# Optimization experiments

Hardware: AMD Instinct MI355X
Metric: run time of the kernel (lower is better)

Reference implementation:

```python
import jax, jax.numpy as jnp
import numpy as np

# static config (matches init_kwargs)
P = 16          # proj_patch_dim (window size)
F = 128         # fmap_dim
NH = F // P     # windows per side = 8
N = P * P       # tokens per window = 256
H = 8           # attn_heads
A = 32          # attn_dim (head dim)
C = 32          # leff_filters_out (channels)
INNER = 128     # leff_filters
B = 8           # batch
EPS = 1e-5

# relative-position index (static)
_c = np.stack(np.meshgrid(np.arange(P), np.arange(P), indexing='ij'))  # [2,P,P]
_f = _c.reshape(2, -1)                                                  # [2,N]
_r = _f[:, :, None] - _f[:, None, :]                                    # [2,N,N]
_rpi = (_r[0] + P - 1) * (2 * P - 1) + (_r[1] + P - 1)                  # [N,N]
RPI = jnp.asarray(_rpi.reshape(-1))

# shifted-window attention mask (static)
_sm = np.zeros((F, F), np.float32)
_cnt = 0
_slices = (slice(0, -P), slice(-P, -P // 2), slice(-P // 2, None))
for _hs in _slices:
    for _ws in _slices:
        _sm[_hs, _ws] = _cnt
        _cnt += 1
_smw = _sm.reshape(NH, P, NH, P).transpose(0, 2, 1, 3).reshape(NH * NH, N)
_am = _smw[:, None, :] - _smw[:, :, None]
_am = np.where(_am != 0, np.float32(-100.0), np.float32(0.0))
SHIFT_MASK = jnp.asarray(_am.reshape(1, NH * NH, 1, N, N))


def _ln(x, g, b):
    m = jnp.mean(x, axis=-1, keepdims=True)
    v = jnp.var(x, axis=-1, keepdims=True)
    return (x - m) / jnp.sqrt(v + EPS) * g + b


def setup_inputs() -> dict:
    key = jax.random.key(0)
    ks = jax.random.split(key, 16)
    s = 0.02
    return {
        'x': jax.random.normal(ks[0], (B, F * F, C), jnp.float32),
        'norm1_g': jnp.ones((C,), jnp.float32),
        'norm1_b': jnp.zeros((C,), jnp.float32),
        'mod_w': jax.random.normal(ks[1], (N, C), jnp.float32) * s,
        'qkv_w': jax.random.normal(ks[2], (C, 3 * H * A), jnp.float32) * s,
        'qkv_b': jnp.zeros((3 * H * A,), jnp.float32),
        'rpbt': jax.random.normal(ks[3], ((2 * P - 1) ** 2, H), jnp.float32) * s,
        'rev_w': jax.random.normal(ks[4], (H * A, C), jnp.float32) * s,
        'rev_b': jnp.zeros((C,), jnp.float32),
        'norm2_g': jnp.ones((C,), jnp.float32),
        'norm2_b': jnp.zeros((C,), jnp.float32),
        'lp1_w': jax.random.normal(ks[5], (C, INNER), jnp.float32) * s,
        'lp1_b': jnp.zeros((INNER,), jnp.float32),
        'conv_w': jax.random.normal(ks[6], (3, 3, INNER, INNER), jnp.float32) * s,  # HWIO
        'conv_b': jnp.zeros((INNER,), jnp.float32),
        'lp2_w': jax.random.normal(ks[7], (INNER, C), jnp.float32) * s,
        'lp2_b': jnp.zeros((C,), jnp.float32),
    }


def reference(x, norm1_g, norm1_b, mod_w, qkv_w, qkv_b, rpbt, rev_w, rev_b,
              norm2_g, norm2_b, lp1_w, lp1_b, conv_w, conv_b, lp2_w, lp2_b):
    shortcut = x
    h = _ln(x, norm1_g, norm1_b)
    h = h.reshape(B, F, F, C)
    h = jnp.roll(h, (-P // 2, -P // 2), axis=(1, 2))          # cyclic shift
    # window partition: [B*NH*NH, N, C]
    h = h.reshape(B, NH, P, NH, P, C).transpose(0, 1, 3, 2, 4, 5).reshape(B * NH * NH, N, C)
    h = h + mod_w                                              # learned modulator
    qkv = h @ qkv_w + qkv_b                                    # [W, N, 3*H*A]
    qkv = qkv.reshape(-1, N, 3, H, A).transpose(2, 0, 3, 1, 4) # [3, W, H, N, A]
    q = qkv[0] * (A ** -0.5)
    k = qkv[1]
    v = qkv[2]
    attn = jnp.einsum('whna,whma->whnm', q, k)                 # [W, H, N, N]
    rpb = rpbt[RPI].reshape(N, N, H).transpose(2, 0, 1)        # [H, N, N]
    attn = attn + rpb[None]
    attn = attn.reshape(B, NH * NH, H, N, N) + SHIFT_MASK
    attn = attn.reshape(-1, H, N, N)
    attn = jax.nn.softmax(attn, axis=-1)
    o = jnp.einsum('whnm,whma->whna', attn, v)                 # [W, H, N, A]
    o = o.transpose(0, 2, 1, 3).reshape(-1, N, H * A)
    o = o @ rev_w + rev_b                                      # [W, N, C]
    # window reverse + reverse cyclic shift
    o = o.reshape(B, NH, NH, P, P, C).transpose(0, 1, 3, 2, 4, 5).reshape(B, F, F, C)
    o = jnp.roll(o, (P // 2, P // 2), axis=(1, 2)).reshape(B, F * F, C)
    x_res = shortcut + o
    # LeFF
    y = _ln(x_res, norm2_g, norm2_b)
    y = jax.nn.gelu(y @ lp1_w + lp1_b, approximate=False)
    y = y.reshape(B, F, F, INNER)
    y = jax.lax.conv_general_dilated(y, conv_w, (1, 1), 'SAME',
                                     dimension_numbers=('NHWC', 'HWIO', 'NHWC')) + conv_b
    y = jax.nn.gelu(y, approximate=False)
    y = y.reshape(B, F * F, INNER)
    y = jax.nn.gelu(y @ lp2_w + lp2_b, approximate=False)
    return y + x_res
```

## Files before the change

### kernel.cpp

```cpp
#include <hip/hip_runtime.h>
#include <math.h>

#define Fdim 128
#define Pw   16
#define Hh   8
#define Cc   32
#define Bb   8

typedef short  short8  __attribute__((ext_vector_type(8)));
typedef float  floatx4 __attribute__((ext_vector_type(4)));

#define QSC   0.17677669529663688f
#define MASKC (-100.0f)

__device__ __forceinline__ float gelu_f(float x){
    return 0.5f * x * (1.0f + erff(x * 0.70710678118654752f));
}
__device__ __forceinline__ unsigned pk2(float a, float b){
    unsigned ua = (__builtin_bit_cast(unsigned, a) + 0x8000u) >> 16;
    unsigned ub = (__builtin_bit_cast(unsigned, b) + 0x8000u) & 0xffff0000u;
    return ua | ub;
}
__device__ __forceinline__ short bf16s(float a){
    return (short)((__builtin_bit_cast(unsigned, a) + 0x8000u) >> 16);
}
__device__ __forceinline__ float hi2f(unsigned d){ return __builtin_bit_cast(float, d & 0xffff0000u); }
__device__ __forceinline__ float lo2f(unsigned d){ return __builtin_bit_cast(float, d << 16); }

__global__ __launch_bounds__(256) void prep_kernel(
    const float* __restrict__ qkv_w, const float* __restrict__ rev_w,
    const float* __restrict__ rpbt,  const float* __restrict__ lp1_w,
    const float* __restrict__ conv_w, const float* __restrict__ lp2_w,
    short* __restrict__ qkv_wT, short* __restrict__ rev_wT, unsigned* __restrict__ rplb,
    short* __restrict__ lp1_wT, short* __restrict__ conv_wT, short* __restrict__ lp2_wT)
{
    int i = blockIdx.x * 256 + threadIdx.x;
    if (i < 24576){
        int col = i >> 5, c = i & 31;
        qkv_wT[i] = bf16s(qkv_w[c*768 + col]);
    } else if (i < 32768){
        int j = i - 24576;
        int h = j >> 10, r = j & 1023;
        int c = r >> 5, a = r & 31;
        rev_wT[j] = bf16s(rev_w[(h*32 + a)*32 + c]);
    } else if (i < 40464){
        int j = i - 32768;
        int h = j / 962, d = j % 962;
        int g0 = (d < 481) ? (2*d) : (2*(d-481) + 1);
        float f0 = (g0     < 961) ? rpbt[g0*8 + h]     : 0.f;
        float f1 = (g0 + 1 < 961) ? rpbt[(g0+1)*8 + h] : 0.f;
        rplb[j] = pk2(f0, f1);
    } else if (i < 44560){
        int j = i - 40464;
        int f = j >> 5, c = j & 31;
        lp1_wT[j] = bf16s(lp1_w[c*128 + f]);
    } else if (i < 192016){
        int j = i - 44560;
        int cil = j & 31, co = (j >> 5) & 127, s = j >> 12;
        int tap = s % 9, kc = s / 9;
        conv_wT[j] = bf16s(conv_w[(tap*128 + kc*32 + cil)*128 + co]);
    } else if (i < 196112){
        int j = i - 192016;
        int oc = j >> 7, co = j & 127;
        lp2_wT[j] = bf16s(lp2_w[co*32 + oc]);
    }
}

__global__ __launch_bounds__(256, 2) void attn_kernel(
    const float* __restrict__ x,   const float* __restrict__ n1g,
    const float* __restrict__ n1b, const float* __restrict__ mod_w,
    const float* __restrict__ qkv_b, const float* __restrict__ rev_b,
    const short* __restrict__ qkv_wT, const short* __restrict__ rev_wT,
    const unsigned* __restrict__ rplb,
    float* __restrict__ x_res)
{
    __shared__ __align__(16) short hmodS[256*32];
    __shared__ __align__(16) short Kbuf[256*40];
    __shared__ __align__(16) short Qbuf[256*40];
    __shared__ __align__(16) short VTb[32*264];
    __shared__ __align__(16) unsigned rplbS[962];
    __shared__ unsigned regnp[64];

    const int w  = blockIdx.x;
    const int b  = w >> 6;
    const int wi = w & 63;
    const int wh = wi >> 3, ww = wi & 7;
    const int tid  = threadIdx.x;
    const int wv   = tid >> 6;
    const int ln   = tid & 63;
    const int quad = ln >> 4;
    const int l15  = ln & 15;
    const bool masked = (wh == 7) || (ww == 7);

    {
        const int n  = tid;
        const int rn = n >> 4, cn = n & 15;
        const int gh = (wh*Pw + rn + 8) & 127;
        const int gw = (ww*Pw + cn + 8) & 127;
        const float* xr = x + (((size_t)b << 14) + (gh << 7) + gw) * Cc;
        float v[Cc];
        const float4* x4 = reinterpret_cast<const float4*>(xr);
        float4* v4 = reinterpret_cast<float4*>(v);
        #pragma unroll
        for (int i = 0; i < Cc/4; i++) v4[i] = x4[i];
        float mean = 0.f;
        #pragma unroll
        for (int c = 0; c < Cc; c++) mean += v[c];
        mean *= (1.0f/Cc);
        float var = 0.f;
        #pragma unroll
        for (int c = 0; c < Cc; c++){ float d = v[c] - mean; var = fmaf(d, d, var); }
        var *= (1.0f/Cc);
        const float rinv = rsqrtf(var + 1e-5f);
        #pragma unroll
        for (int c = 0; c < Cc; c++)
            v[c] = (v[c] - mean)*rinv*n1g[c] + n1b[c] + mod_w[n*Cc + c];
        #pragma unroll
        for (int i = 0; i < 4; i++){
            uint4 dw;
            dw.x = pk2(v[8*i+0], v[8*i+1]);
            dw.y = pk2(v[8*i+2], v[8*i+3]);
            dw.z = pk2(v[8*i+4], v[8*i+5]);
            dw.w = pk2(v[8*i+6], v[8*i+7]);
            *(uint4*)(&hmodS[n*32 + i*8]) = dw;
        }
    }
    if (tid < 64){
        int rm  = tid >> 2;
        int shm = wh*Pw + rm;
        int hreg = (shm < 112) ? 0 : ((shm < 120) ? 1 : 2);
        unsigned dw = 0;
        #pragma unroll
        for (int i = 0; i < 4; i++){
            int cm  = (tid & 3)*4 + i;
            int swm = ww*Pw + cm;
            int wreg = (swm < 112) ? 0 : ((swm < 120) ? 1 : 2);
            dw |= (unsigned)(hreg*3 + wreg) << (8*i);
        }
        regnp[tid] = dw;
    }
    __syncthreads();

    unsigned regq[4] = {0,0,0,0};
    if (masked){
        #pragma unroll
        for (int nt = 0; nt < 4; nt++){
            int q = wv*64 + nt*16 + l15;
            regq[nt] = (regnp[q >> 2] >> ((q & 3)*8)) & 255u;
        }
    }

    floatx4 RV[2][4];
    #pragma unroll
    for (int cm = 0; cm < 2; cm++)
        #pragma unroll
        for (int nt = 0; nt < 4; nt++)
            RV[cm][nt] = (floatx4){0.f,0.f,0.f,0.f};

    const int s0lane = 12 + l15 - 4*quad;
    const floatx4 zz = (floatx4){0.f,0.f,0.f,0.f};

    for (int h = 0; h < Hh; h++){
        __syncthreads();

        #pragma unroll
        for (int k2 = 0; k2 < 4; k2++){
            int i = k2*256 + tid;
            if (i < 962) rplbS[i] = rplb[h*962 + i];
        }

        short8 HA[4];
        #pragma unroll
        for (int i = 0; i < 4; i++)
            HA[i] = *(const short8*)(&hmodS[(wv*64 + i*16 + l15)*32 + quad*8]);
        short8 WB[3][2]; float bias[3][2];
        #pragma unroll
        for (int m = 0; m < 3; m++)
            #pragma unroll
            for (int nt = 0; nt < 2; nt++){
                int col = m*256 + h*32 + nt*16 + l15;
                WB[m][nt]  = *(const short8*)(qkv_wT + col*32 + quad*8);
                bias[m][nt] = qkv_b[col];
            }
        #pragma unroll
        for (int i = 0; i < 4; i++){
            int tokbase = wv*64 + i*16 + quad*4;
            #pragma unroll
            for (int nt = 0; nt < 2; nt++){
                int col = nt*16 + l15;
                floatx4 qf = __builtin_amdgcn_mfma_f32_16x16x32_bf16(HA[i], WB[0][nt], zz, 0,0,0);
                floatx4 kf = __builtin_amdgcn_mfma_f32_16x16x32_bf16(HA[i], WB[1][nt], zz, 0,0,0);
                floatx4 vf = __builtin_amdgcn_mfma_f32_16x16x32_bf16(HA[i], WB[2][nt], zz, 0,0,0);
                float bq = bias[0][nt], bk = bias[1][nt], bv = bias[2][nt];
                #pragma unroll
                for (int r = 0; r < 4; r++){
                    Qbuf[(tokbase + r)*40 + col] = bf16s((qf[r] + bq)*QSC);
                    Kbuf[(tokbase + r)*40 + col] = bf16s(kf[r] + bk);
                }
                uint2 vv;
                vv.x = pk2(vf[0] + bv, vf[1] + bv);
                vv.y = pk2(vf[2] + bv, vf[3] + bv);
                *(uint2*)(&VTb[col*264 + tokbase]) = vv;
            }
        }
        __syncthreads();

        short8 QB[4];
        #pragma unroll
        for (int nt = 0; nt < 4; nt++)
            QB[nt] = *(const short8*)(&Qbuf[(wv*64 + nt*16 + l15)*40 + quad*8]);

        floatx4 OT[2][4];
        #pragma unroll
        for (int am = 0; am < 2; am++)
            #pragma unroll
            for (int nt = 0; nt < 4; nt++)
                OT[am][nt] = (floatx4){0.f,0.f,0.f,0.f};
        float rs[4] = {0.f,0.f,0.f,0.f};

        for (int ch = 0; ch < 8; ch++){
            short8 KA[2];
            KA[0] = *(const short8*)(&Kbuf[(ch*32 +      l15)*40 + quad*8]);
            KA[1] = *(const short8*)(&Kbuf[(ch*32 + 16 + l15)*40 + quad*8]);

            unsigned pd0[5], pd1[5];
            int base = wv*4 - ch*2;
            #pragma unroll
            for (int j = 0; j < 5; j++){
                int dt  = base + j - 1;
                int g0  = (dt + 15)*31 + s0lane;
                int dwi = (g0 & 1) ? (481 + (g0 >> 1)) : (g0 >> 1);
                pd0[j] = rplbS[dwi];
                pd1[j] = rplbS[dwi + 1];
            }
            unsigned rk[2] = {0,0};
            if (masked){
                rk[0] = regnp[ch*8 +     quad];
                rk[1] = regnp[ch*8 + 4 + quad];
            }

            floatx4 S[2][4];
            #pragma unroll
            for (int sub = 0; sub < 2; sub++)
                #pragma unroll
                for (int nt = 0; nt < 4; nt++)
                    S[sub][nt] = __builtin_amdgcn_mfma_f32_16x16x32_bf16(KA[sub], QB[nt], zz, 0,0,0);

            #pragma unroll
            for (int sub = 0; sub < 2; sub++)
                #pragma unroll
                for (int nt = 0; nt < 4; nt++){
                    int j = nt - sub + 1;
                    float e0 = S[sub][nt][0] + hi2f(pd1[j]);
                    float e1 = S[sub][nt][1] + lo2f(pd1[j]);
                    float e2 = S[sub][nt][2] + hi2f(pd0[j]);
                    float e3 = S[sub][nt][3] + lo2f(pd0[j]);
                    if (masked){
                        e0 += (((rk[sub]      ) & 255u) == regq[nt]) ? 0.f : MASKC;
                        e1 += (((rk[sub] >>  8) & 255u) == regq[nt]) ? 0.f : MASKC;
                        e2 += (((rk[sub] >> 16) & 255u) == regq[nt]) ? 0.f : MASKC;
                        e3 += (((rk[sub] >> 24) & 255u) == regq[nt]) ? 0.f : MASKC;
                    }
                    float p0 = __expf(e0), p1 = __expf(e1);
                    float p2 = __expf(e2), p3 = __expf(e3);
                    rs[nt] += (p0 + p1) + (p2 + p3);
                    uint2 pv; pv.x = pk2(p0, p1); pv.y = pk2(p2, p3);
                    *(uint2*)(&Qbuf[(wv*64 + nt*16 + l15)*40 + sub*16 + quad*4]) = pv;
                }

            short8 VA0 = *(const short8*)(&VTb[(     l15)*264 + ch*32 + quad*8]);
            short8 VA1 = *(const short8*)(&VTb[(16 + l15)*264 + ch*32 + quad*8]);
            #pragma unroll
            for (int nt = 0; nt < 4; nt++){
                short8 PB = *(const short8*)(&Qbuf[(wv*64 + nt*16 + l15)*40 + quad*8]);
                OT[0][nt] = __builtin_amdgcn_mfma_f32_16x16x32_bf16(VA0, PB, OT[0][nt], 0,0,0);
                OT[1][nt] = __builtin_amdgcn_mfma_f32_16x16x32_bf16(VA1, PB, OT[1][nt], 0,0,0);
            }
        }

        float inv[4];
        #pragma unroll
        for (int nt = 0; nt < 4; nt++){
            float t = rs[nt] + __shfl_xor(rs[nt], 16, 64);
            t = t + __shfl_xor(t, 32, 64);
            inv[nt] = 1.0f / t;
        }
        #pragma unroll
        for (int am = 0; am < 2; am++)
            #pragma unroll
            for (int nt = 0; nt < 4; nt++){
                floatx4 o = OT[am][nt];
                float iv = inv[nt];
                uint2 ov;
                ov.x = pk2(o[0]*iv, o[1]*iv);
                ov.y = pk2(o[2]*iv, o[3]*iv);
                *(uint2*)(&Qbuf[(wv*64 + nt*16 + l15)*40 + am*16 + quad*4]) = ov;
            }

        short8 RA0 = *(const short8*)(rev_wT + h*1024 + (     l15)*32 + quad*8);
        short8 RA1 = *(const short8*)(rev_wT + h*1024 + (16 + l15)*32 + quad*8);
        #pragma unroll
        for (int nt = 0; nt < 4; nt++){
            short8 OB = *(const short8*)(&Qbuf[(wv*64 + nt*16 + l15)*40 + quad*8]);
            RV[0][nt] = __builtin_amdgcn_mfma_f32_16x16x32_bf16(RA0, OB, RV[0][nt], 0,0,0);
            RV[1][nt] = __builtin_amdgcn_mfma_f32_16x16x32_bf16(RA1, OB, RV[1][nt], 0,0,0);
        }
    }

    #pragma unroll
    for (int cm = 0; cm < 2; cm++){
        float4 rb = *(const float4*)(rev_b + cm*16 + quad*4);
        #pragma unroll
        for (int nt = 0; nt < 4; nt++){
            int gh = (wh*Pw + wv*4 + nt + 8) & 127;
            int gw = (ww*Pw + l15 + 8) & 127;
            size_t gaddr = (((size_t)b << 14) + (gh << 7) + gw)*Cc + cm*16 + quad*4;
            float4 xv = *(const float4*)(x + gaddr);
            floatx4 o = RV[cm][nt];
            float4 ov;
            ov.x = xv.x + rb.x + o[0];
            ov.y = xv.y + rb.y + o[1];
            ov.z = xv.z + rb.z + o[2];
            ov.w = xv.w + rb.w + o[3];
            *(float4*)(x_res + gaddr) = ov;
        }
    }
}

__global__ __launch_bounds__(256, 2) void leff_kernel(
    const float* __restrict__ x_res, const float* __restrict__ n2g,
    const float* __restrict__ n2b,  const float* __restrict__ lp1_b,
    const float* __restrict__ conv_b, const float* __restrict__ lp2_b,
    const short* __restrict__ lp1_wT, const short* __restrict__ conv_wT,
    const short* __restrict__ lp2_wT, float* __restrict__ out)
{
    __shared__ __align__(16) char lds[74240];
    short* xa   = (short*)lds;
    short* y1c  = (short*)(lds + 26880);
    short* wbuf = (short*)(lds + 53760);
    short* y2   = (short*)lds;

    const int blk = blockIdx.x;
    const int b   = blk >> 6;
    const int ty  = (blk >> 3) & 7, tx = blk & 7;
    const int tid  = threadIdx.x;
    const int wv   = tid >> 6;
    const int ln   = tid & 63;
    const int quad = ln >> 4;
    const int l15  = ln & 15;
    const floatx4 zz = (floatx4){0.f,0.f,0.f,0.f};

    for (int hp = tid; hp < 336; hp += 256){
        int hy = hp / 18, hx = hp - hy*18;
        int gy = ty*16 + hy - 1, gx = tx*16 + hx - 1;
        bool ok = (hp < 324) && ((unsigned)gy < 128u) && ((unsigned)gx < 128u);
        if (ok){
            const float* xr = x_res + (((size_t)b << 14) + (gy << 7) + gx)*Cc;
            float v[Cc];
            const float4* x4 = reinterpret_cast<const float4*>(xr);
            float4* v4 = reinterpret_cast<float4*>(v);
            #pragma unroll
            for (int i = 0; i < Cc/4; i++) v4[i] = x4[i];
            float mean = 0.f;
            #pragma unroll
            for (int c = 0; c < Cc; c++) mean += v[c];
            mean *= (1.0f/Cc);
            float var = 0.f;
            #pragma unroll
            for (int c = 0; c < Cc; c++){ float d = v[c] - mean; var = fmaf(d, d, var); }
            var *= (1.0f/Cc);
            const float rinv = rsqrtf(var + 1e-5f);
            #pragma unroll
            for (int i = 0; i < 4; i++){
                float w0 = (v[8*i+0]-mean)*rinv*n2g[8*i+0] + n2b[8*i+0];
                float w1 = (v[8*i+1]-mean)*rinv*n2g[8*i+1] + n2b[8*i+1];
                float w2 = (v[8*i+2]-mean)*rinv*n2g[8*i+2] + n2b[8*i+2];
                float w3 = (v[8*i+3]-mean)*rinv*n2g[8*i+3] + n2b[8*i+3];
                float w4 = (v[8*i+4]-mean)*rinv*n2g[8*i+4] + n2b[8*i+4];
                float w5 = (v[8*i+5]-mean)*rinv*n2g[8*i+5] + n2b[8*i+5];
                float w6 = (v[8*i+6]-mean)*rinv*n2g[8*i+6] + n2b[8*i+6];
                float w7 = (v[8*i+7]-mean)*rinv*n2g[8*i+7] + n2b[8*i+7];
                uint4 dw;
                dw.x = pk2(w0,w1); dw.y = pk2(w2,w3);
                dw.z = pk2(w4,w5); dw.w = pk2(w6,w7);
                *(uint4*)(xa + hp*40 + i*8) = dw;
            }
        } else {
            uint4 z = {0,0,0,0};
            #pragma unroll
            for (int i = 0; i < 4; i++) *(uint4*)(xa + hp*40 + i*8) = z;
        }
    }

    {
        const uint4* s = (const uint4*)(conv_wT);
        uint4 a0 = s[tid*2], a1 = s[tid*2 + 1];
        ((uint4*)wbuf)[tid*2]     = a0;
        ((uint4*)wbuf)[tid*2 + 1] = a1;
    }

    floatx4 acc[4][8];
    #pragma unroll
    for (int j = 0; j < 4; j++)
        #pragma unroll
        for (int m = 0; m < 8; m++) acc[j][m] = zz;

    for (int idx = 0; idx < 36; idx++){
        const int kc  = idx / 9;
        const int tap = idx - kc*9;

        if (tap == 0){
            __syncthreads();
            short8 A1[2]; float4 b1[2];
            #pragma unroll
            for (int mt = 0; mt < 2; mt++){
                A1[mt] = *(const short8*)(lp1_wT + (kc*32 + mt*16 + l15)*32 + quad*8);
                b1[mt] = *(const float4*)(lp1_b + kc*32 + mt*16 + quad*4);
            }
            #pragma unroll
            for (int ii = 0; ii < 6; ii++){
                int nt = wv + 4*ii;
                if (nt < 21){
                    int px = nt*16 + l15;
                    int hy = px / 18, hx = px - hy*18;
                    int gy = ty*16 + hy - 1, gx = tx*16 + hx - 1;
                    bool oob = (px >= 324) || ((unsigned)gy > 127u) || ((unsigned)gx > 127u);
                    short8 Bx = *(const short8*)(xa + px*40 + quad*8);
                    #pragma unroll
                    for (int mt = 0; mt < 2; mt++){
                        floatx4 c = __builtin_amdgcn_mfma_f32_16x16x32_bf16(A1[mt], Bx, zz, 0,0,0);
                        float v0 = oob ? 0.f : gelu_f(c[0] + b1[mt].x);
                        float v1 = oob ? 0.f : gelu_f(c[1] + b1[mt].y);
                        float v2 = oob ? 0.f : gelu_f(c[2] + b1[mt].z);
                        float v3 = oob ? 0.f : gelu_f(c[3] + b1[mt].w);
                        uint2 pv; pv.x = pk2(v0, v1); pv.y = pk2(v2, v3);
                        *(uint2*)(y1c + px*40 + mt*16 + quad*4) = pv;
                    }
                }
            }
        }

        uint4 pf0, pf1;
        if (idx < 35){
            const uint4* s = (const uint4*)((const char*)conv_wT + (size_t)(idx+1)*8192);
            pf0 = s[tid*2]; pf1 = s[tid*2 + 1];
        }

        __syncthreads();

        const short* wb = wbuf + (idx & 1)*4096;
        const int ky = tap / 3, kx = tap - ky*3;

        short8 Aw[8];
        #pragma unroll
        for (int m = 0; m < 8; m++)
            Aw[m] = *(const short8*)(wb + (m*16 + l15)*32 + quad*8);

        #pragma unroll
        for (int j = 0; j < 4; j++){
            int oy = wv*4 + j;
            int hp = (oy + ky)*18 + kx + l15;
            short8 Bf = *(const short8*)(y1c + hp*40 + quad*8);
            #pragma unroll
            for (int m = 0; m < 8; m++)
                acc[j][m] = __builtin_amdgcn_mfma_f32_16x16x32_bf16(Aw[m], Bf, acc[j][m], 0,0,0);
        }

        if (idx < 35){
            short* wn = wbuf + ((idx + 1) & 1)*4096;
            ((uint4*)wn)[tid*2]     = pf0;
            ((uint4*)wn)[tid*2 + 1] = pf1;
        }
    }

    __syncthreads();

    #pragma unroll
    for (int j = 0; j < 4; j++){
        int px = (wv*4 + j)*16 + l15;
        #pragma unroll
        for (int m = 0; m < 8; m++){
            float4 cb = *(const float4*)(conv_b + m*16 + quad*4);
            floatx4 a = acc[j][m];
            float v0 = gelu_f(a[0] + cb.x);
            float v1 = gelu_f(a[1] + cb.y);
            float v2 = gelu_f(a[2] + cb.z);
            float v3 = gelu_f(a[3] + cb.w);
            uint2 pv; pv.x = pk2(v0, v1); pv.y = pk2(v2, v3);
            *(uint2*)(y2 + px*136 + m*16 + quad*4) = pv;
        }
    }
    __syncthreads();

    short8 A2[2][4]; float4 lb[2];
    #pragma unroll
    for (int mt = 0; mt < 2; mt++){
        #pragma unroll
        for (int k = 0; k < 4; k++)
            A2[mt][k] = *(const short8*)(lp2_wT + (mt*16 + l15)*128 + k*32 + quad*8);
        lb[mt] = *(const float4*)(lp2_b + mt*16 + quad*4);
    }
    #pragma unroll
    for (int j = 0; j < 4; j++){
        int oy = wv*4 + j;
        floatx4 c2[2] = {zz, zz};
        #pragma unroll
        for (int k = 0; k < 4; k++){
            short8 Bf = *(const short8*)(y2 + (oy*16 + l15)*136 + k*32 + quad*8);
            c2[0] = __builtin_amdgcn_mfma_f32_16x16x32_bf16(A2[0][k], Bf, c2[0], 0,0,0);
            c2[1] = __builtin_amdgcn_mfma_f32_16x16x32_bf16(A2[1][k], Bf, c2[1], 0,0,0);
        }
        int gy = ty*16 + oy, gx = tx*16 + l15;
        size_t base = (((size_t)b << 14) + (gy << 7) + gx)*Cc;
        #pragma unroll
        for (int mt = 0; mt < 2; mt++){
            size_t ad = base + mt*16 + quad*4;
            float4 xr = *(const float4*)(x_res + ad);
            float4 ov;
            ov.x = gelu_f(c2[mt][0] + lb[mt].x) + xr.x;
            ov.y = gelu_f(c2[mt][1] + lb[mt].y) + xr.y;
            ov.z = gelu_f(c2[mt][2] + lb[mt].z) + xr.z;
            ov.w = gelu_f(c2[mt][3] + lb[mt].w) + xr.w;
            *(float4*)(out + ad) = ov;
        }
    }
}

extern "C" void kernel_launch(void* const* d_in, const int* in_sizes, int n_in,
                              void* d_out, int out_size, void* d_ws, size_t ws_size,
                              hipStream_t stream)
{
    (void)in_sizes; (void)n_in; (void)out_size; (void)ws_size;
    const float* x      = (const float*)d_in[0];
    const float* n1g    = (const float*)d_in[1];
    const float* n1b    = (const float*)d_in[2];
    const float* mod_w  = (const float*)d_in[3];
    const float* qkv_w  = (const float*)d_in[4];
    const float* qkv_b  = (const float*)d_in[5];
    const float* rpbt   = (const float*)d_in[6];
    const float* rev_w  = (const float*)d_in[7];
    const float* rev_b  = (const float*)d_in[8];
    const float* n2g    = (const float*)d_in[9];
    const float* n2b    = (const float*)d_in[10];
    const float* lp1_w  = (const float*)d_in[11];
    const float* lp1_b  = (const float*)d_in[12];
    const float* conv_w = (const float*)d_in[13];
    const float* conv_b = (const float*)d_in[14];
    const float* lp2_w  = (const float*)d_in[15];
    const float* lp2_b  = (const float*)d_in[16];
    float* out = (float*)d_out;

    char* wsb = (char*)d_ws;
    float*    x_res  = (float*)wsb;
    short*    qkv_wT = (short*)(wsb + 16777216);
    short*    rev_wT = (short*)(wsb + 16826368);
    unsigned* rplbT  = (unsigned*)(wsb + 16842752);
    short*    lp1_wT = (short*)(wsb + 16873536);
    short*    conv_wT= (short*)(wsb + 16881728);
    short*    lp2_wT = (short*)(wsb + 17176640);

    prep_kernel<<<767, 256, 0, stream>>>(qkv_w, rev_w, rpbt, lp1_w, conv_w, lp2_w,
                                         qkv_wT, rev_wT, rplbT, lp1_wT, conv_wT, lp2_wT);
    attn_kernel<<<512, 256, 0, stream>>>(x, n1g, n1b, mod_w, qkv_b, rev_b,
                                         qkv_wT, rev_wT, rplbT, x_res);
    leff_kernel<<<512, 256, 0, stream>>>(x_res, n2g, n2b, lp1_b, conv_b, lp2_b,
                                         lp1_wT, conv_wT, lp2_wT, out);
}
```

Measured before the change: 292.3 us.

## Double block size to 512 threads and use exp2 softmax with split-K LDS layouts

Both the attention and LeFF kernels now run 512 threads (8 waves) per block, so each wave handles half as many token/row tiles and the per-thread accumulators shrink. The hmod and conv-weight LDS layouts are reorganised into k-chunk-major order so each quad reads a contiguous 8-element slice. Softmax switches from __expf to exp2f, with log2(e) folded into the query scale, the relative-position bias table and the mask constant. The aim is more waves for latency hiding and lower register pressure, at the cost of more barrier participants and less per-wave reuse of weight fragments.

```diff
diff --git a/kernel.cpp b/kernel.cpp
--- a/kernel.cpp
+++ b/kernel.cpp
@@ -10,8 +10,8 @@
 typedef short  short8  __attribute__((ext_vector_type(8)));
 typedef float  floatx4 __attribute__((ext_vector_type(4)));
 
-#define QSC   0.17677669529663688f
-#define MASKC (-100.0f)
+#define QSCL   0.2550348637f
+#define MASKC2 (-144.26950408889634f)
 
 __device__ __forceinline__ float gelu_f(float x){
     return 0.5f * x * (1.0f + erff(x * 0.70710678118654752f));
@@ -47,8 +47,8 @@
         int j = i - 32768;
         int h = j / 962, d = j % 962;
         int g0 = (d < 481) ? (2*d) : (2*(d-481) + 1);
-        float f0 = (g0     < 961) ? rpbt[g0*8 + h]     : 0.f;
-        float f1 = (g0 + 1 < 961) ? rpbt[(g0+1)*8 + h] : 0.f;
+        float f0 = (g0     < 961) ? rpbt[g0*8 + h]*1.4426950408889634f : 0.f;
+        float f1 = (g0 + 1 < 961) ? rpbt[(g0+1)*8 + h]*1.4426950408889634f : 0.f;
         rplb[j] = pk2(f0, f1);
     } else if (i < 44560){
         int j = i - 40464;
@@ -56,9 +56,12 @@
         lp1_wT[j] = bf16s(lp1_w[c*128 + f]);
     } else if (i < 192016){
         int j = i - 44560;
-        int cil = j & 31, co = (j >> 5) & 127, s = j >> 12;
+        int ci_in = j & 7;
+        int co    = (j >> 3) & 127;
+        int chk   = (j >> 10) & 3;
+        int s     = j >> 12;
         int tap = s % 9, kc = s / 9;
-        conv_wT[j] = bf16s(conv_w[(tap*128 + kc*32 + cil)*128 + co]);
+        conv_wT[j] = bf16s(conv_w[(tap*128 + kc*32 + chk*8 + ci_in)*128 + co]);
     } else if (i < 196112){
         int j = i - 192016;
         int oc = j >> 7, co = j & 127;
@@ -66,7 +69,7 @@
     }
 }
 
-__global__ __launch_bounds__(256, 2) void attn_kernel(
+__global__ __launch_bounds__(512, 4) void attn_kernel(
     const float* __restrict__ x,   const float* __restrict__ n1g,
     const float* __restrict__ n1b, const float* __restrict__ mod_w,
     const float* __restrict__ qkv_b, const float* __restrict__ rev_b,
@@ -74,7 +77,7 @@
     const unsigned* __restrict__ rplb,
     float* __restrict__ x_res)
 {
-    __shared__ __align__(16) short hmodS[256*32];
+    __shared__ __align__(16) short hmodS[4*256*8];
     __shared__ __align__(16) short Kbuf[256*40];
     __shared__ __align__(16) short Qbuf[256*40];
     __shared__ __align__(16) short VTb[32*264];
@@ -92,7 +95,7 @@
     const int l15  = ln & 15;
     const bool masked = (wh == 7) || (ww == 7);
 
-    {
+    if (tid < 256){
         const int n  = tid;
         const int rn = n >> 4, cn = n & 15;
         const int gh = (wh*Pw + rn + 8) & 127;
@@ -122,7 +125,7 @@
             dw.y = pk2(v[8*i+2], v[8*i+3]);
             dw.z = pk2(v[8*i+4], v[8*i+5]);
             dw.w = pk2(v[8*i+6], v[8*i+7]);
-            *(uint4*)(&hmodS[n*32 + i*8]) = dw;
+            *(uint4*)(&hmodS[i*2048 + n*8]) = dw;
         }
     }
     if (tid < 64){
@@ -141,20 +144,20 @@
     }
     __syncthreads();
 
-    unsigned regq[4] = {0,0,0,0};
+    unsigned regq[2] = {0,0};
     if (masked){
         #pragma unroll
-        for (int nt = 0; nt < 4; nt++){
-            int q = wv*64 + nt*16 + l15;
+        for (int nt = 0; nt < 2; nt++){
+            int q = wv*32 + nt*16 + l15;
             regq[nt] = (regnp[q >> 2] >> ((q & 3)*8)) & 255u;
         }
     }
 
-    floatx4 RV[2][4];
+    floatx4 RV[2][2];
     #pragma unroll
     for (int cm = 0; cm < 2; cm++)
         #pragma unroll
-        for (int nt = 0; nt < 4; nt++)
+        for (int nt = 0; nt < 2; nt++)
             RV[cm][nt] = (floatx4){0.f,0.f,0.f,0.f};
 
     const int s0lane = 12 + l15 - 4*quad;
@@ -164,15 +167,15 @@
         __syncthreads();
 
         #pragma unroll
-        for (int k2 = 0; k2 < 4; k2++){
-            int i = k2*256 + tid;
+        for (int k2 = 0; k2 < 2; k2++){
+            int i = k2*512 + tid;
             if (i < 962) rplbS[i] = rplb[h*962 + i];
         }
 
-        short8 HA[4];
-        #pragma unroll
-        for (int i = 0; i < 4; i++)
-            HA[i] = *(const short8*)(&hmodS[(wv*64 + i*16 + l15)*32 + quad*8]);
+        short8 HA[2];
+        #pragma unroll
+        for (int ii = 0; ii < 2; ii++)
+            HA[ii] = *(const short8*)(&hmodS[quad*2048 + (wv*32 + ii*16 + l15)*8]);
         short8 WB[3][2]; float bias[3][2];
         #pragma unroll
         for (int m = 0; m < 3; m++)
@@ -183,18 +186,18 @@
                 bias[m][nt] = qkv_b[col];
             }
         #pragma unroll
-        for (int i = 0; i < 4; i++){
-            int tokbase = wv*64 + i*16 + quad*4;
+        for (int ii = 0; ii < 2; ii++){
+            int tokbase = wv*32 + ii*16 + quad*4;
             #pragma unroll
             for (int nt = 0; nt < 2; nt++){
                 int col = nt*16 + l15;
-                floatx4 qf = __builtin_amdgcn_mfma_f32_16x16x32_bf16(HA[i], WB[0][nt], zz, 0,0,0);
-                floatx4 kf = __builtin_amdgcn_mfma_f32_16x16x32_bf16(HA[i], WB[1][nt], zz, 0,0,0);
-                floatx4 vf = __builtin_amdgcn_mfma_f32_16x16x32_bf16(HA[i], WB[2][nt], zz, 0,0,0);
+                floatx4 qf = __builtin_amdgcn_mfma_f32_16x16x32_bf16(HA[ii], WB[0][nt], zz, 0,0,0);
+                floatx4 kf = __builtin_amdgcn_mfma_f32_16x16x32_bf16(HA[ii], WB[1][nt], zz, 0,0,0);
+                floatx4 vf = __builtin_amdgcn_mfma_f32_16x16x32_bf16(HA[ii], WB[2][nt], zz, 0,0,0);
                 float bq = bias[0][nt], bk = bias[1][nt], bv = bias[2][nt];
                 #pragma unroll
                 for (int r = 0; r < 4; r++){
-                    Qbuf[(tokbase + r)*40 + col] = bf16s((qf[r] + bq)*QSC);
+                    Qbuf[(tokbase + r)*40 + col] = bf16s((qf[r] + bq)*QSCL);
                     Kbuf[(tokbase + r)*40 + col] = bf16s(kf[r] + bk);
                 }
                 uint2 vv;
@@ -205,28 +208,28 @@
         }
         __syncthreads();
 
-        short8 QB[4];
-        #pragma unroll
-        for (int nt = 0; nt < 4; nt++)
-            QB[nt] = *(const short8*)(&Qbuf[(wv*64 + nt*16 + l15)*40 + quad*8]);
-
-        floatx4 OT[2][4];
+        short8 QB[2];
+        #pragma unroll
+        for (int nt = 0; nt < 2; nt++)
+            QB[nt] = *(const short8*)(&Qbuf[(wv*32 + nt*16 + l15)*40 + quad*8]);
+
+        floatx4 OT[2][2];
         #pragma unroll
         for (int am = 0; am < 2; am++)
             #pragma unroll
-            for (int nt = 0; nt < 4; nt++)
+            for (int nt = 0; nt < 2; nt++)
                 OT[am][nt] = (floatx4){0.f,0.f,0.f,0.f};
-        float rs[4] = {0.f,0.f,0.f,0.f};
+        float rs[2] = {0.f,0.f};
 
         for (int ch = 0; ch < 8; ch++){
             short8 KA[2];
             KA[0] = *(const short8*)(&Kbuf[(ch*32 +      l15)*40 + quad*8]);
             KA[1] = *(const short8*)(&Kbuf[(ch*32 + 16 + l15)*40 + quad*8]);
 
-            unsigned pd0[5], pd1[5];
-            int base = wv*4 - ch*2;
-            #pragma unroll
-            for (int j = 0; j < 5; j++){
+            unsigned pd0[3], pd1[3];
+            int base = wv*2 - ch*2;
+            #pragma unroll
+            for (int j = 0; j < 3; j++){
                 int dt  = base + j - 1;
                 int g0  = (dt + 15)*31 + s0lane;
                 int dwi = (g0 & 1) ? (481 + (g0 >> 1)) : (g0 >> 1);
@@ -239,48 +242,48 @@
                 rk[1] = regnp[ch*8 + 4 + quad];
             }
 
-            floatx4 S[2][4];
+            floatx4 S[2][2];
             #pragma unroll
             for (int sub = 0; sub < 2; sub++)
                 #pragma unroll
-                for (int nt = 0; nt < 4; nt++)
+                for (int nt = 0; nt < 2; nt++)
                     S[sub][nt] = __builtin_amdgcn_mfma_f32_16x16x32_bf16(KA[sub], QB[nt], zz, 0,0,0);
 
             #pragma unroll
             for (int sub = 0; sub < 2; sub++)
                 #pragma unroll
-                for (int nt = 0; nt < 4; nt++){
+                for (int nt = 0; nt < 2; nt++){
                     int j = nt - sub + 1;
                     float e0 = S[sub][nt][0] + hi2f(pd1[j]);
                     float e1 = S[sub][nt][1] + lo2f(pd1[j]);
                     float e2 = S[sub][nt][2] + hi2f(pd0[j]);
                     float e3 = S[sub][nt][3] + lo2f(pd0[j]);
                     if (masked){
-                        e0 += (((rk[sub]      ) & 255u) == regq[nt]) ? 0.f : MASKC;
-                        e1 += (((rk[sub] >>  8) & 255u) == regq[nt]) ? 0.f : MASKC;
-                        e2 += (((rk[sub] >> 16) & 255u) == regq[nt]) ? 0.f : MASKC;
-                        e3 += (((rk[sub] >> 24) & 255u) == regq[nt]) ? 0.f : MASKC;
+                        e0 += (((rk[sub]      ) & 255u) == regq[nt]) ? 0.f : MASKC2;
+                        e1 += (((rk[sub] >>  8) & 255u) == regq[nt]) ? 0.f : MASKC2;
+                        e2 += (((rk[sub] >> 16) & 255u) == regq[nt]) ? 0.f : MASKC2;
+                        e3 += (((rk[sub] >> 24) & 255u) == regq[nt]) ? 0.f : MASKC2;
                     }
-                    float p0 = __expf(e0), p1 = __expf(e1);
-                    float p2 = __expf(e2), p3 = __expf(e3);
+                    float p0 = exp2f(e0), p1 = exp2f(e1);
+                    float p2 = exp2f(e2), p3 = exp2f(e3);
                     rs[nt] += (p0 + p1) + (p2 + p3);
                     uint2 pv; pv.x = pk2(p0, p1); pv.y = pk2(p2, p3);
-                    *(uint2*)(&Qbuf[(wv*64 + nt*16 + l15)*40 + sub*16 + quad*4]) = pv;
+                    *(uint2*)(&Qbuf[(wv*32 + nt*16 + l15)*40 + sub*16 + quad*4]) = pv;
                 }
 
             short8 VA0 = *(const short8*)(&VTb[(     l15)*264 + ch*32 + quad*8]);
             short8 VA1 = *(const short8*)(&VTb[(16 + l15)*264 + ch*32 + quad*8]);
             #pragma unroll
-            for (int nt = 0; nt < 4; nt++){
-                short8 PB = *(const short8*)(&Qbuf[(wv*64 + nt*16 + l15)*40 + quad*8]);
+            for (int nt = 0; nt < 2; nt++){
+                short8 PB = *(const short8*)(&Qbuf[(wv*32 + nt*16 + l15)*40 + quad*8]);
                 OT[0][nt] = __builtin_amdgcn_mfma_f32_16x16x32_bf16(VA0, PB, OT[0][nt], 0,0,0);
                 OT[1][nt] = __builtin_amdgcn_mfma_f32_16x16x32_bf16(VA1, PB, OT[1][nt], 0,0,0);
             }
         }
 
-        float inv[4];
-        #pragma unroll
-        for (int nt = 0; nt < 4; nt++){
+        float inv[2];
+        #pragma unroll
+        for (int nt = 0; nt < 2; nt++){
             float t = rs[nt] + __shfl_xor(rs[nt], 16, 64);
             t = t + __shfl_xor(t, 32, 64);
             inv[nt] = 1.0f / t;
@@ -288,20 +291,20 @@
         #pragma unroll
         for (int am = 0; am < 2; am++)
             #pragma unroll
-            for (int nt = 0; nt < 4; nt++){
+            for (int nt = 0; nt < 2; nt++){
                 floatx4 o = OT[am][nt];
                 float iv = inv[nt];
                 uint2 ov;
                 ov.x = pk2(o[0]*iv, o[1]*iv);
                 ov.y = pk2(o[2]*iv, o[3]*iv);
-                *(uint2*)(&Qbuf[(wv*64 + nt*16 + l15)*40 + am*16 + quad*4]) = ov;
+                *(uint2*)(&Qbuf[(wv*32 + nt*16 + l15)*40 + am*16 + quad*4]) = ov;
             }
 
         short8 RA0 = *(const short8*)(rev_wT + h*1024 + (     l15)*32 + quad*8);
         short8 RA1 = *(const short8*)(rev_wT + h*1024 + (16 + l15)*32 + quad*8);
         #pragma unroll
-        for (int nt = 0; nt < 4; nt++){
-            short8 OB = *(const short8*)(&Qbuf[(wv*64 + nt*16 + l15)*40 + quad*8]);
+        for (int nt = 0; nt < 2; nt++){
+            short8 OB = *(const short8*)(&Qbuf[(wv*32 + nt*16 + l15)*40 + quad*8]);
             RV[0][nt] = __builtin_amdgcn_mfma_f32_16x16x32_bf16(RA0, OB, RV[0][nt], 0,0,0);
             RV[1][nt] = __builtin_amdgcn_mfma_f32_16x16x32_bf16(RA1, OB, RV[1][nt], 0,0,0);
         }
@@ -311,8 +314,8 @@
     for (int cm = 0; cm < 2; cm++){
         float4 rb = *(const float4*)(rev_b + cm*16 + quad*4);
         #pragma unroll
-        for (int nt = 0; nt < 4; nt++){
-            int gh = (wh*Pw + wv*4 + nt + 8) & 127;
+        for (int nt = 0; nt < 2; nt++){
+            int gh = (wh*Pw + wv*2 + nt + 8) & 127;
             int gw = (ww*Pw + l15 + 8) & 127;
             size_t gaddr = (((size_t)b << 14) + (gh << 7) + gw)*Cc + cm*16 + quad*4;
             float4 xv = *(const float4*)(x + gaddr);
@@ -327,14 +330,14 @@
     }
 }
 
-__global__ __launch_bounds__(256, 2) void leff_kernel(
+__global__ __launch_bounds__(512, 4) void leff_kernel(
     const float* __restrict__ x_res, const float* __restrict__ n2g,
     const float* __restrict__ n2b,  const float* __restrict__ lp1_b,
     const float* __restrict__ conv_b, const float* __restrict__ lp2_b,
     const short* __restrict__ lp1_wT, const short* __restrict__ conv_wT,
     const short* __restrict__ lp2_wT, float* __restrict__ out)
 {
-    __shared__ __align__(16) char lds[74240];
+    __shared__ __align__(16) char lds[70144];
     short* xa   = (short*)lds;
     short* y1c  = (short*)(lds + 26880);
     short* wbuf = (short*)(lds + 53760);
@@ -350,7 +353,8 @@
     const int l15  = ln & 15;
     const floatx4 zz = (floatx4){0.f,0.f,0.f,0.f};
 
-    for (int hp = tid; hp < 336; hp += 256){
+    if (tid < 336){
+        int hp = tid;
         int hy = hp / 18, hx = hp - hy*18;
         int gy = ty*16 + hy - 1, gx = tx*16 + hx - 1;
         bool ok = (hp < 324) && ((unsigned)gy < 128u) && ((unsigned)gx < 128u);
@@ -392,16 +396,11 @@
         }
     }
 
-    {
-        const uint4* s = (const uint4*)(conv_wT);
-        uint4 a0 = s[tid*2], a1 = s[tid*2 + 1];
-        ((uint4*)wbuf)[tid*2]     = a0;
-        ((uint4*)wbuf)[tid*2 + 1] = a1;
-    }
-
-    floatx4 acc[4][8];
+    ((uint4*)wbuf)[tid] = ((const uint4*)conv_wT)[tid];
+
+    floatx4 acc[2][8];
     #pragma unroll
-    for (int j = 0; j < 4; j++)
+    for (int j = 0; j < 2; j++)
         #pragma unroll
         for (int m = 0; m < 8; m++) acc[j][m] = zz;
 
@@ -418,8 +417,8 @@
                 b1[mt] = *(const float4*)(lp1_b + kc*32 + mt*16 + quad*4);
             }
             #pragma unroll
-            for (int ii = 0; ii < 6; ii++){
-                int nt = wv + 4*ii;
+            for (int ii = 0; ii < 3; ii++){
+                int nt = wv + 8*ii;
                 if (nt < 21){
                     int px = nt*16 + l15;
                     int hy = px / 18, hx = px - hy*18;
@@ -440,44 +439,37 @@
             }
         }
 
-        uint4 pf0, pf1;
-        if (idx < 35){
-            const uint4* s = (const uint4*)((const char*)conv_wT + (size_t)(idx+1)*8192);
-            pf0 = s[tid*2]; pf1 = s[tid*2 + 1];
-        }
+        uint4 pf;
+        if (idx < 35) pf = ((const uint4*)conv_wT)[(idx + 1)*512 + tid];
 
         __syncthreads();
 
         const short* wb = wbuf + (idx & 1)*4096;
         const int ky = tap / 3, kx = tap - ky*3;
 
-        short8 Aw[8];
-        #pragma unroll
-        for (int m = 0; m < 8; m++)
-            Aw[m] = *(const short8*)(wb + (m*16 + l15)*32 + quad*8);
-
-        #pragma unroll
-        for (int j = 0; j < 4; j++){
-            int oy = wv*4 + j;
+        short8 Bf[2];
+        #pragma unroll
+        for (int j = 0; j < 2; j++){
+            int oy = wv*2 + j;
             int hp = (oy + ky)*18 + kx + l15;
-            short8 Bf = *(const short8*)(y1c + hp*40 + quad*8);
-            #pragma unroll
-            for (int m = 0; m < 8; m++)
-                acc[j][m] = __builtin_amdgcn_mfma_f32_16x16x32_bf16(Aw[m], Bf, acc[j][m], 0,0,0);
-        }
-
-        if (idx < 35){
-            short* wn = wbuf + ((idx + 1) & 1)*4096;
-            ((uint4*)wn)[tid*2]     = pf0;
-            ((uint4*)wn)[tid*2 + 1] = pf1;
-        }
+            Bf[j] = *(const short8*)(y1c + hp*40 + quad*8);
+        }
+        #pragma unroll
+        for (int m = 0; m < 8; m++){
+            short8 Aw = *(const short8*)(wb + quad*1024 + (m*16 + l15)*8);
+            acc[0][m] = __builtin_amdgcn_mfma_f32_16x16x32_bf16(Aw, Bf[0], acc[0][m], 0,0,0);
+            acc[1][m] = __builtin_amdgcn_mfma_f32_16x16x32_bf16(Aw, Bf[1], acc[1][m], 0,0,0);
+        }
+
+        if (idx < 35)
+            ((uint4*)(wbuf + ((idx + 1) & 1)*4096))[tid] = pf;
     }
 
     __syncthreads();
 
     #pragma unroll
-    for (int j = 0; j < 4; j++){
-        int px = (wv*4 + j)*16 + l15;
+    for (int j = 0; j < 2; j++){
+        int px = (wv*2 + j)*16 + l15;
         #pragma unroll
         for (int m = 0; m < 8; m++){
             float4 cb = *(const float4*)(conv_b + m*16 + quad*4);
@@ -501,8 +493,8 @@
         lb[mt] = *(const float4*)(lp2_b + mt*16 + quad*4);
     }
     #pragma unroll
-    for (int j = 0; j < 4; j++){
-        int oy = wv*4 + j;
+    for (int j = 0; j < 2; j++){
+        int oy = wv*2 + j;
         floatx4 c2[2] = {zz, zz};
         #pragma unroll
         for (int k = 0; k < 4; k++){
@@ -561,8 +553,8 @@
 
     prep_kernel<<<767, 256, 0, stream>>>(qkv_w, rev_w, rpbt, lp1_w, conv_w, lp2_w,
                                          qkv_wT, rev_wT, rplbT, lp1_wT, conv_wT, lp2_wT);
-    attn_kernel<<<512, 256, 0, stream>>>(x, n1g, n1b, mod_w, qkv_b, rev_b,
+    attn_kernel<<<512, 512, 0, stream>>>(x, n1g, n1b, mod_w, qkv_b, rev_b,
                                          qkv_wT, rev_wT, rplbT, x_res);
-    leff_kernel<<<512, 256, 0, stream>>>(x_res, n2g, n2b, lp1_b, conv_b, lp2_b,
+    leff_kernel<<<512, 512, 0, stream>>>(x_res, n2g, n2b, lp1_b, conv_b, lp2_b,
                                          lp1_wT, conv_wT, lp2_wT, out);
 }
```

Result: no change. 289.7 us (-0.9%).
